# Performance work log

Hardware: AMD Instinct MI355X
Metric: run time of the kernel (lower is better)

The kernel has to match this reference:

```python
import jax, jax.numpy as jnp
import numpy as np

D_MODEL = 512
N_HEADS = 8
D_K = D_MODEL // N_HEADS
D_FF = 2048
N = 4096
EPS = 1e-5


def _layer_norm(x, g, b):
    mu = jnp.mean(x, axis=-1, keepdims=True)
    var = jnp.mean(jnp.square(x - mu), axis=-1, keepdims=True)
    return (x - mu) * jax.lax.rsqrt(var + EPS) * g + b


def setup_inputs() -> dict:
    key = jax.random.key(0)
    ks = jax.random.split(key, 16)
    s = 1.0 / np.sqrt(D_MODEL)
    sf = 1.0 / np.sqrt(D_FF)
    inp = {
        "h": jax.random.normal(ks[0], (N, D_MODEL), dtype=jnp.float32),
        "adj": jax.random.randint(ks[1], (N, N), 0, 2, dtype=jnp.int32),
        "Wq": jax.random.uniform(ks[2], (D_MODEL, D_MODEL), jnp.float32, -s, s),
        "bq": jnp.zeros((D_MODEL,), jnp.float32),
        "Wk": jax.random.uniform(ks[3], (D_MODEL, D_MODEL), jnp.float32, -s, s),
        "bk": jnp.zeros((D_MODEL,), jnp.float32),
        "Wv": jax.random.uniform(ks[4], (D_MODEL, D_MODEL), jnp.float32, -s, s),
        "bv": jnp.zeros((D_MODEL,), jnp.float32),
        "Wo": jax.random.uniform(ks[5], (D_MODEL, D_MODEL), jnp.float32, -s, s),
        "bo": jnp.zeros((D_MODEL,), jnp.float32),
        "W1": jax.random.uniform(ks[6], (D_FF, D_MODEL), jnp.float32, -s, s),
        "b1": jnp.zeros((D_FF,), jnp.float32),
        "W2": jax.random.uniform(ks[7], (D_MODEL, D_FF), jnp.float32, -sf, sf),
        "b2": jnp.zeros((D_MODEL,), jnp.float32),
        "ln1_g": jnp.ones((D_MODEL,), jnp.float32),
        "ln1_b": jnp.zeros((D_MODEL,), jnp.float32),
        "ln2_g": jnp.ones((D_MODEL,), jnp.float32),
        "ln2_b": jnp.zeros((D_MODEL,), jnp.float32),
    }
    return inp


def reference(h, adj, Wq, bq, Wk, bk, Wv, bv, Wo, bo, W1, b1, W2, b2,
              ln1_g, ln1_b, ln2_g, ln2_b):
    n = h.shape[0]
    # adjacency + self loops, used as attention mask (batch=1)
    mask = adj.astype(jnp.float32) + jnp.eye(n, dtype=jnp.float32)  # [N,N]

    # QKV projections, split into heads: [N, H, Dk]
    q = (h @ Wq.T + bq).reshape(n, N_HEADS, D_K)
    k = (h @ Wk.T + bk).reshape(n, N_HEADS, D_K)
    v = (h @ Wv.T + bv).reshape(n, N_HEADS, D_K)

    scores = jnp.einsum("nhd,mhd->hnm", q, k) / jnp.sqrt(jnp.float32(D_K))
    scores = jnp.where(mask[None, :, :] == 0, jnp.float32(-1e9), scores)
    attn = jax.nn.softmax(scores, axis=-1)  # dropout is identity in eval
    ctx = jnp.einsum("hnm,mhd->nhd", attn, v).reshape(n, D_MODEL)
    attn_out = ctx @ Wo.T + bo

    h1 = _layer_norm(h + attn_out, ln1_g, ln1_b)
    ff = jax.nn.relu(h1 @ W1.T + b1) @ W2.T + b2
    h2 = _layer_norm(h1 + ff, ln2_g, ln2_b)
    return h2
```

## Files before the change

kernel.cpp:

```cpp
#include <hip/hip_runtime.h>
#include <stdint.h>
#include <stddef.h>

typedef __bf16 bf16;
typedef __bf16 bf16x8 __attribute__((ext_vector_type(8)));
typedef float  f32x4  __attribute__((ext_vector_type(4)));

typedef __attribute__((address_space(3))) void       lds_void;
typedef __attribute__((address_space(1))) const void gbl_cvoid;

#define ASYNC_CP16(g, l) \
  __builtin_amdgcn_global_load_lds((gbl_cvoid*)(g), (lds_void*)(l), 16, 0, 0)

__device__ __forceinline__ int swz(int r) { return (r & 7) ^ ((r & 8) >> 1); }

struct CastArgs {
  const float* src[7];
  bf16*        dst[7];
  int          cum[8];
};

__global__ __launch_bounds__(256) void k_cast(CastArgs a, int total8)
{
  const int g = blockIdx.x * 256 + threadIdx.x;
  if (g >= total8) return;
  int t = 0;
  while (a.cum[t + 1] <= g) ++t;
  const int i = g - a.cum[t];
  const float4* s = (const float4*)(a.src[t]) + (size_t)i * 2;
  const float4 x0 = s[0], x1 = s[1];
  bf16x8 y;
  y[0] = (bf16)x0.x; y[1] = (bf16)x0.y; y[2] = (bf16)x0.z; y[3] = (bf16)x0.w;
  y[4] = (bf16)x1.x; y[5] = (bf16)x1.y; y[6] = (bf16)x1.z; y[7] = (bf16)x1.w;
  *(bf16x8*)(a.dst[t] + (size_t)i * 8) = y;
}

__device__ __forceinline__ void gemm_core_async(
    const bf16* __restrict__ A, const bf16* __restrict__ B,
    bf16* As, bf16* Bs, f32x4 (&acc)[4][4],
    int K, int m0, int n0, int kbeg, int kend)
{
  const int tid    = threadIdx.x;
  const int lane   = tid & 63;
  const int wave   = tid >> 6;
  const int lane15 = lane & 15;
  const int quad   = lane >> 4;
  const int wm     = (wave & 1) << 6;
  const int wn     = (wave >> 1) << 6;

  int srow[4], soff[4];
#pragma unroll
  for (int i = 0; i < 4; ++i) {
    int c   = ((wave * 4 + i) << 6) + lane;
    srow[i] = c >> 3;
    soff[i] = ((c & 7) ^ swz(srow[i])) * 8;
  }

  const bf16* Ab = A + (size_t)m0 * K;
  const bf16* Bb = B + (size_t)n0 * K;

  for (int k0 = kbeg; k0 < kend; k0 += 64) {
#pragma unroll
    for (int i = 0; i < 4; ++i) {
      ASYNC_CP16(Ab + (size_t)srow[i] * K + k0 + soff[i], &As[(wave * 4 + i) * 512]);
      ASYNC_CP16(Bb + (size_t)srow[i] * K + k0 + soff[i], &Bs[(wave * 4 + i) * 512]);
    }
    __syncthreads();

#pragma unroll
    for (int kk = 0; kk < 2; ++kk) {
      bf16x8 af[4], bfr[4];
#pragma unroll
      for (int f = 0; f < 4; ++f) {
        const int ra = wm + f * 16 + lane15;
        af[f]  = *(const bf16x8*)&As[ra * 64 + (((kk * 4 + quad) ^ swz(ra)) * 8)];
        const int rb = wn + f * 16 + lane15;
        bfr[f] = *(const bf16x8*)&Bs[rb * 64 + (((kk * 4 + quad) ^ swz(rb)) * 8)];
      }
#pragma unroll
      for (int fm = 0; fm < 4; ++fm)
#pragma unroll
        for (int fn = 0; fn < 4; ++fn)
          acc[fm][fn] = __builtin_amdgcn_mfma_f32_16x16x32_bf16(
              af[fm], bfr[fn], acc[fm][fn], 0, 0, 0);
    }
    __syncthreads();
  }
}

__global__ __launch_bounds__(256, 2) void k_gemm(
    const bf16* __restrict__ A, const bf16* __restrict__ B,
    const float* __restrict__ bias, bf16* __restrict__ C,
    int N, int K, int relu)
{
  __shared__ __align__(16) bf16 As[128 * 64];
  __shared__ __align__(16) bf16 Bs[128 * 64];
  const int m0 = blockIdx.x * 128, n0 = blockIdx.y * 128;
  f32x4 acc[4][4] = {};
  gemm_core_async(A, B, As, Bs, acc, K, m0, n0, 0, K);

  const int lane15 = threadIdx.x & 15;
  const int quad   = (threadIdx.x & 63) >> 4;
  const int wave   = threadIdx.x >> 6;
  const int wm     = (wave & 1) << 6, wn = (wave >> 1) << 6;
#pragma unroll
  for (int fm = 0; fm < 4; ++fm)
#pragma unroll
    for (int fn = 0; fn < 4; ++fn) {
      const int col = n0 + wn + fn * 16 + lane15;
      const float bv = bias[col];
#pragma unroll
      for (int r = 0; r < 4; ++r) {
        const int row = m0 + wm + fm * 16 + quad * 4 + r;
        float v = acc[fm][fn][r] + bv;
        if (relu) v = fmaxf(v, 0.0f);
        C[(size_t)row * N + col] = (bf16)v;
      }
    }
}

__global__ __launch_bounds__(256, 2) void k_gemm_qkv(
    const bf16* __restrict__ h,
    const bf16* __restrict__ Wq, const bf16* __restrict__ Wk, const bf16* __restrict__ Wv,
    const float* __restrict__ bq, const float* __restrict__ bk, const float* __restrict__ bv,
    bf16* __restrict__ q, bf16* __restrict__ k, bf16* __restrict__ v)
{
  __shared__ __align__(16) bf16 As[128 * 64];
  __shared__ __align__(16) bf16 Bs[128 * 64];
  const bf16* B; const float* bias; bf16* C;
  if (blockIdx.z == 0)      { B = Wq; bias = bq; C = q; }
  else if (blockIdx.z == 1) { B = Wk; bias = bk; C = k; }
  else                      { B = Wv; bias = bv; C = v; }
  const int m0 = blockIdx.x * 128, n0 = blockIdx.y * 128;
  f32x4 acc[4][4] = {};
  gemm_core_async(h, B, As, Bs, acc, 512, m0, n0, 0, 512);

  const int lane15 = threadIdx.x & 15;
  const int quad   = (threadIdx.x & 63) >> 4;
  const int wave   = threadIdx.x >> 6;
  const int wm     = (wave & 1) << 6, wn = (wave >> 1) << 6;
#pragma unroll
  for (int fm = 0; fm < 4; ++fm)
#pragma unroll
    for (int fn = 0; fn < 4; ++fn) {
      const int col = n0 + wn + fn * 16 + lane15;
      const float bv = bias[col];
#pragma unroll
      for (int r = 0; r < 4; ++r) {
        const int row = m0 + wm + fm * 16 + quad * 4 + r;
        C[(size_t)row * 512 + col] = (bf16)(acc[fm][fn][r] + bv);
      }
    }
}

__global__ __launch_bounds__(256, 2) void k_gemm_sk(
    const bf16* __restrict__ A, const bf16* __restrict__ B,
    float* __restrict__ Cp, int N, int K, int Ksplit)
{
  __shared__ __align__(16) bf16 As[128 * 64];
  __shared__ __align__(16) bf16 Bs[128 * 64];
  const int m0 = blockIdx.x * 128, n0 = blockIdx.y * 128;
  const int kbeg = blockIdx.z * Ksplit;
  f32x4 acc[4][4] = {};
  gemm_core_async(A, B, As, Bs, acc, K, m0, n0, kbeg, kbeg + Ksplit);

  const int lane15 = threadIdx.x & 15;
  const int quad   = (threadIdx.x & 63) >> 4;
  const int wave   = threadIdx.x >> 6;
  const int wm     = (wave & 1) << 6, wn = (wave >> 1) << 6;
  float* Cz = Cp + (size_t)blockIdx.z * 4096 * N;
#pragma unroll
  for (int fm = 0; fm < 4; ++fm)
#pragma unroll
    for (int fn = 0; fn < 4; ++fn) {
      const int col = n0 + wn + fn * 16 + lane15;
#pragma unroll
      for (int r = 0; r < 4; ++r) {
        const int row = m0 + wm + fm * 16 + quad * 4 + r;
        Cz[(size_t)row * N + col] = acc[fm][fn][r];
      }
    }
}

__global__ __launch_bounds__(256) void k_packmask(
    const int* __restrict__ adj, unsigned long long* __restrict__ mb)
{
  const int gw   = (int)((blockIdx.x * 256 + threadIdx.x) >> 6);
  const int lane = threadIdx.x & 63;
  const int a    = adj[(size_t)gw * 64 + lane];
  unsigned long long m = __ballot(a != 0);
  const int row = gw >> 6, wc = gw & 63;
  if ((row >> 6) == wc) m |= 1ull << (row & 63);
  if (lane == 0) mb[gw] = m;
}

__global__ __launch_bounds__(256) void k_transpose_v(
    const bf16* __restrict__ v, bf16* __restrict__ vt)
{
  __shared__ __align__(16) bf16 T[64 * 72];
  const int r0 = blockIdx.x * 64;
  const int c0 = blockIdx.y * 64;
  const int tid = threadIdx.x;
#pragma unroll
  for (int rr = 0; rr < 2; ++rr) {
    int idx = rr * 256 + tid;
    int kr = idx >> 3, ch = (idx & 7) * 8;
    *(bf16x8*)&T[kr * 72 + ch] = *(const bf16x8*)&v[(size_t)(r0 + kr) * 512 + c0 + ch];
  }
  __syncthreads();
#pragma unroll
  for (int rr = 0; rr < 2; ++rr) {
    int idx = rr * 256 + tid;
    int cr = idx >> 3, ch = idx & 7;
    bf16x8 y;
#pragma unroll
    for (int j = 0; j < 8; ++j) y[j] = T[(ch * 8 + j) * 72 + cr];
    *(bf16x8*)&vt[(size_t)(c0 + cr) * 4096 + r0 + ch * 8] = y;
  }
}

__global__ __launch_bounds__(256, 4) void k_attn(
    const bf16* __restrict__ Q, const bf16* __restrict__ Km,
    const bf16* __restrict__ Vt, const unsigned long long* __restrict__ mb,
    bf16* __restrict__ Opart, float* __restrict__ Lpart)
{
  __shared__ __align__(16) bf16 Ks[64 * 72];
  __shared__ __align__(16) bf16 Vs[64 * 72];
  __shared__ __align__(16) bf16 Plb[4][32 * 72];

  const int tid    = threadIdx.x;
  const int wave   = tid >> 6;
  const int lane   = tid & 63;
  const int lane15 = lane & 15;
  const int quad   = lane >> 4;
  const int sp     = blockIdx.x & 3;
  const int hd     = (blockIdx.x >> 2) & 7;
  const int qt     = blockIdx.x >> 5;
  const int qrow   = qt * 128 + wave * 32;

  bf16x8 qf[2][2];
#pragma unroll
  for (int mt = 0; mt < 2; ++mt)
#pragma unroll
    for (int c = 0; c < 2; ++c)
      qf[mt][c] = *(const bf16x8*)&Q[(size_t)(qrow + mt * 16 + lane15) * 512 +
                                     hd * 64 + c * 32 + quad * 8];

  bf16x8 ones;
#pragma unroll
  for (int j = 0; j < 8; ++j) ones[j] = (bf16)1.0f;

  f32x4 o[2][4] = {};
  f32x4 la[2]   = {};

  for (int kt = sp * 16; kt < sp * 16 + 16; ++kt) {
    const int kb = kt * 64;
#pragma unroll
    for (int rr = 0; rr < 2; ++rr) {
      int idx = rr * 256 + tid;
      int a = idx >> 3, ch = (idx & 7) * 8;
      *(bf16x8*)&Ks[a * 72 + ch] = *(const bf16x8*)&Km[(size_t)(kb + a) * 512 + hd * 64 + ch];
      *(bf16x8*)&Vs[a * 72 + ch] = *(const bf16x8*)&Vt[(size_t)(hd * 64 + a) * 4096 + kb + ch];
    }
    __syncthreads();

    unsigned long long mw[2][4];
#pragma unroll
    for (int mt = 0; mt < 2; ++mt)
#pragma unroll
      for (int r = 0; r < 4; ++r)
        mw[mt][r] = mb[(size_t)(qrow + mt * 16 + quad * 4 + r) * 64 + kt] >> lane15;

#pragma unroll
    for (int g = 0; g < 4; ++g) {
      bf16x8 k0f = *(const bf16x8*)&Ks[(g * 16 + lane15) * 72 + quad * 8];
      bf16x8 k1f = *(const bf16x8*)&Ks[(g * 16 + lane15) * 72 + 32 + quad * 8];
#pragma unroll
      for (int mt = 0; mt < 2; ++mt) {
        f32x4 s = {};
        s = __builtin_amdgcn_mfma_f32_16x16x32_bf16(qf[mt][0], k0f, s, 0, 0, 0);
        s = __builtin_amdgcn_mfma_f32_16x16x32_bf16(qf[mt][1], k1f, s, 0, 0, 0);
#pragma unroll
        for (int r = 0; r < 4; ++r) {
          const bool ok = ((mw[mt][r] >> (g * 16)) & 1ull) != 0;
          const float p = ok ? __expf(s[r] * 0.125f) : 0.0f;
          Plb[wave][(mt * 16 + quad * 4 + r) * 72 + g * 16 + lane15] = (bf16)p;
        }
      }
    }

#pragma unroll
    for (int c2 = 0; c2 < 2; ++c2) {
      bf16x8 vf[4];
#pragma unroll
      for (int g2 = 0; g2 < 4; ++g2)
        vf[g2] = *(const bf16x8*)&Vs[(g2 * 16 + lane15) * 72 + c2 * 32 + quad * 8];
#pragma unroll
      for (int mt = 0; mt < 2; ++mt) {
        bf16x8 pa = *(const bf16x8*)&Plb[wave][(mt * 16 + lane15) * 72 + c2 * 32 + quad * 8];
        la[mt] = __builtin_amdgcn_mfma_f32_16x16x32_bf16(pa, ones, la[mt], 0, 0, 0);
#pragma unroll
        for (int g2 = 0; g2 < 4; ++g2)
          o[mt][g2] = __builtin_amdgcn_mfma_f32_16x16x32_bf16(pa, vf[g2], o[mt][g2], 0, 0, 0);
      }
    }
    __syncthreads();
  }

  bf16* Oz = Opart + (size_t)sp * 4096 * 512;
#pragma unroll
  for (int mt = 0; mt < 2; ++mt) {
#pragma unroll
    for (int g2 = 0; g2 < 4; ++g2)
#pragma unroll
      for (int r = 0; r < 4; ++r) {
        const int row = qrow + mt * 16 + quad * 4 + r;
        Oz[(size_t)row * 512 + hd * 64 + g2 * 16 + lane15] = (bf16)o[mt][g2][r];
      }
    if (lane15 == 0) {
#pragma unroll
      for (int r = 0; r < 4; ++r)
        Lpart[sp * 32768 + (qrow + mt * 16 + quad * 4 + r) * 8 + hd] = la[mt][r];
    }
  }
}

__global__ __launch_bounds__(256) void k_attn_combine(
    const bf16* __restrict__ Opart, const float* __restrict__ Lpart,
    bf16* __restrict__ ctx)
{
  const int g = blockIdx.x * 256 + threadIdx.x;
  const size_t base = (size_t)g * 8;
  const int row = g >> 6;
  const int hd  = (g & 63) >> 3;
  float acc[8] = {};
  float l = 0.0f;
#pragma unroll
  for (int s = 0; s < 4; ++s) {
    bf16x8 ov = *(const bf16x8*)&Opart[(size_t)s * 4096 * 512 + base];
#pragma unroll
    for (int j = 0; j < 8; ++j) acc[j] += (float)ov[j];
    l += Lpart[s * 32768 + row * 8 + hd];
  }
  const float rl = 1.0f / l;
  bf16x8 y;
#pragma unroll
  for (int j = 0; j < 8; ++j) y[j] = (bf16)(acc[j] * rl);
  *(bf16x8*)(ctx + base) = y;
}

template <int F32OUT>
__global__ __launch_bounds__(256) void k_addln_sk(
    const bf16* __restrict__ x, const float* __restrict__ Cp,
    const float* __restrict__ bias,
    const float* __restrict__ gam, const float* __restrict__ bet,
    void* __restrict__ out)
{
  const int wave = threadIdx.x >> 6, lane = threadIdx.x & 63;
  const int row  = blockIdx.x * 4 + wave;
  const size_t base = (size_t)row * 512 + lane * 8;
  const int col = lane * 8;
  bf16x8 xv = *(const bf16x8*)(x + base);
  const float* p0 = Cp + base;
  const float* p1 = Cp + (size_t)4096 * 512 + base;
  f32x4 a0 = *(const f32x4*)p0, a1 = *(const f32x4*)(p0 + 4);
  f32x4 b0 = *(const f32x4*)p1, b1 = *(const f32x4*)(p1 + 4);
  f32x4 c0 = *(const f32x4*)(bias + col), c1 = *(const f32x4*)(bias + col + 4);
  float v[8], s = 0.0f, s2 = 0.0f;
#pragma unroll
  for (int j = 0; j < 4; ++j) {
    v[j]     = (float)xv[j]     + a0[j] + b0[j] + c0[j];
    v[4 + j] = (float)xv[4 + j] + a1[j] + b1[j] + c1[j];
  }
#pragma unroll
  for (int j = 0; j < 8; ++j) { s += v[j]; s2 += v[j] * v[j]; }
#pragma unroll
  for (int d = 1; d < 64; d <<= 1) { s += __shfl_xor(s, d, 64); s2 += __shfl_xor(s2, d, 64); }
  const float mu  = s * (1.0f / 512.0f);
  const float var = s2 * (1.0f / 512.0f) - mu * mu;
  const float rs  = rsqrtf(var + 1e-5f);
  f32x4 g0 = *(const f32x4*)(gam + col), g1 = *(const f32x4*)(gam + col + 4);
  f32x4 e0 = *(const f32x4*)(bet + col), e1 = *(const f32x4*)(bet + col + 4);
  if (F32OUT) {
    float* o = (float*)out + base;
#pragma unroll
    for (int j = 0; j < 4; ++j) {
      o[j]     = ((v[j] - mu) * rs) * g0[j] + e0[j];
      o[4 + j] = ((v[4 + j] - mu) * rs) * g1[j] + e1[j];
    }
  } else {
    bf16x8 ov;
#pragma unroll
    for (int j = 0; j < 4; ++j) {
      ov[j]     = (bf16)(((v[j] - mu) * rs) * g0[j] + e0[j]);
      ov[4 + j] = (bf16)(((v[4 + j] - mu) * rs) * g1[j] + e1[j]);
    }
    *(bf16x8*)((bf16*)out + base) = ov;
  }
}

extern "C" void kernel_launch(void* const* d_in, const int* in_sizes, int n_in,
                              void* d_out, int out_size, void* d_ws, size_t ws_size,
                              hipStream_t stream)
{
  const int*   adj = (const int*)  d_in[1];
  const float* bq  = (const float*)d_in[3];
  const float* bk  = (const float*)d_in[5];
  const float* bv  = (const float*)d_in[7];
  const float* bo  = (const float*)d_in[9];
  const float* b1  = (const float*)d_in[11];
  const float* b2  = (const float*)d_in[13];
  const float* g1  = (const float*)d_in[14];
  const float* be1 = (const float*)d_in[15];
  const float* g2  = (const float*)d_in[16];
  const float* be2 = (const float*)d_in[17];

  char* ws = (char*)d_ws;
  const size_t MB = 1024 * 1024;

  bf16* hb  = (bf16*)(ws + 0 * MB);
  bf16* Wqb = (bf16*)(ws + 4 * MB);
  bf16* Wkb = (bf16*)(ws + 4 * MB + 512 * 1024);
  bf16* Wvb = (bf16*)(ws + 5 * MB);
  bf16* Wob = (bf16*)(ws + 5 * MB + 512 * 1024);
  bf16* W1b = (bf16*)(ws + 6 * MB);
  bf16* W2b = (bf16*)(ws + 8 * MB);

  bf16* q    = (bf16*)(ws + 12 * MB);
  bf16* k    = (bf16*)(ws + 16 * MB);
  bf16* v    = (bf16*)(ws + 20 * MB);
  bf16* vt   = (bf16*)(ws + 24 * MB);
  unsigned long long* mbits = (unsigned long long*)(ws + 28 * MB);
  bf16* ctx  = (bf16*)(ws + 30 * MB);
  bf16*  Opart = (bf16*)(ws + 34 * MB);
  float* Lpart = (float*)(ws + 50 * MB);
  float* skP   = (float*)(ws + 34 * MB);
  bf16* h1   = (bf16*)(ws + 12 * MB);
  bf16* ff1  = (bf16*)(ws + 16 * MB);

  CastArgs ca;
  const int srcIdx[7] = {0, 2, 4, 6, 8, 10, 12};
  bf16* dsts[7] = {hb, Wqb, Wkb, Wvb, Wob, W1b, W2b};
  int cum = 0;
  for (int t = 0; t < 7; ++t) {
    ca.src[t] = (const float*)d_in[srcIdx[t]];
    ca.dst[t] = dsts[t];
    ca.cum[t] = cum;
    cum += in_sizes[srcIdx[t]] / 8;
  }
  ca.cum[7] = cum;

  const dim3 blk(256);
  k_cast<<<dim3((cum + 255) / 256), blk, 0, stream>>>(ca, cum);

  k_gemm_qkv<<<dim3(32, 4, 3), blk, 0, stream>>>(hb, Wqb, Wkb, Wvb, bq, bk, bv, q, k, v);
  k_transpose_v<<<dim3(64, 8), blk, 0, stream>>>(v, vt);
  k_packmask<<<dim3(65536), blk, 0, stream>>>(adj, mbits);
  k_attn<<<dim3(1024), blk, 0, stream>>>(q, k, vt, mbits, Opart, Lpart);
  k_attn_combine<<<dim3(1024), blk, 0, stream>>>(Opart, Lpart, ctx);
  k_gemm_sk<<<dim3(32, 4, 2), blk, 0, stream>>>(ctx, Wob, skP, 512, 512, 256);
  k_addln_sk<0><<<dim3(1024), blk, 0, stream>>>(hb, skP, bo, g1, be1, (void*)h1);
  k_gemm<<<dim3(32, 16), blk, 0, stream>>>(h1, W1b, b1, ff1, 2048, 512, 1);
  k_gemm_sk<<<dim3(32, 4, 2), blk, 0, stream>>>(ff1, W2b, skP, 512, 2048, 1024);
  k_addln_sk<1><<<dim3(1024), blk, 0, stream>>>(h1, skP, b2, g2, be2, d_out);
}
```

Before: 311.8 us.

## Fuse prep kernels, fold V transpose into QKV GEMM, use async loads in attention

Merges the mask packing and fp32->bf16 cast into one launch. Treats Wq/Wk/Wv as one concatenated weight matrix (relying on their contiguous workspace layout) in a 64-row-tile QKV GEMM whose V epilogue writes the transposed V directly, which removes the separate transpose kernel. The split-K GEMMs move to 64-row tiles with higher occupancy, and attention now loads K/V tiles into swizzled LDS with async global-to-LDS copies. Together these cut launch count and extra global traffic, at the cost of smaller tiles with less reuse.

```diff
diff --git a/kernel.cpp b/kernel.cpp
--- a/kernel.cpp
+++ b/kernel.cpp
@@ -20,40 +20,62 @@
   int          cum[8];
 };
 
-__global__ __launch_bounds__(256) void k_cast(CastArgs a, int total8)
-{
-  const int g = blockIdx.x * 256 + threadIdx.x;
-  if (g >= total8) return;
-  int t = 0;
-  while (a.cum[t + 1] <= g) ++t;
-  const int i = g - a.cum[t];
-  const float4* s = (const float4*)(a.src[t]) + (size_t)i * 2;
-  const float4 x0 = s[0], x1 = s[1];
-  bf16x8 y;
-  y[0] = (bf16)x0.x; y[1] = (bf16)x0.y; y[2] = (bf16)x0.z; y[3] = (bf16)x0.w;
-  y[4] = (bf16)x1.x; y[5] = (bf16)x1.y; y[6] = (bf16)x1.z; y[7] = (bf16)x1.w;
-  *(bf16x8*)(a.dst[t] + (size_t)i * 8) = y;
-}
-
+__global__ __launch_bounds__(256) void k_prep(
+    const int* __restrict__ adj, unsigned long long* __restrict__ mb,
+    CastArgs a, int total8)
+{
+  const int bid = blockIdx.x;
+  if (bid < 65536) {
+    const int gw   = (int)(((unsigned)bid * 256 + threadIdx.x) >> 6);
+    const int lane = threadIdx.x & 63;
+    const int av   = adj[(size_t)gw * 64 + lane];
+    unsigned long long m = __ballot(av != 0);
+    const int row = gw >> 6, wc = gw & 63;
+    if ((row >> 6) == wc) m |= 1ull << (row & 63);
+    if (lane == 0) mb[gw] = m;
+  } else {
+    const int g = (bid - 65536) * 256 + threadIdx.x;
+    if (g >= total8) return;
+    int t = 0;
+    while (a.cum[t + 1] <= g) ++t;
+    const int i = g - a.cum[t];
+    const float4* s = (const float4*)(a.src[t]) + (size_t)i * 2;
+    const float4 x0 = s[0], x1 = s[1];
+    bf16x8 y;
+    y[0] = (bf16)x0.x; y[1] = (bf16)x0.y; y[2] = (bf16)x0.z; y[3] = (bf16)x0.w;
+    y[4] = (bf16)x1.x; y[5] = (bf16)x1.y; y[6] = (bf16)x1.z; y[7] = (bf16)x1.w;
+    *(bf16x8*)(a.dst[t] + (size_t)i * 8) = y;
+  }
+}
+
+template <int MT>
 __device__ __forceinline__ void gemm_core_async(
     const bf16* __restrict__ A, const bf16* __restrict__ B,
-    bf16* As, bf16* Bs, f32x4 (&acc)[4][4],
+    bf16* As, bf16* Bs, f32x4 (&acc)[4][(MT == 128) ? 4 : 2],
     int K, int m0, int n0, int kbeg, int kend)
 {
+  constexpr int FN = (MT == 128) ? 4 : 2;
+  constexpr int IA = MT / 32;
   const int tid    = threadIdx.x;
   const int lane   = tid & 63;
   const int wave   = tid >> 6;
   const int lane15 = lane & 15;
   const int quad   = lane >> 4;
-  const int wm     = (wave & 1) << 6;
-  const int wn     = (wave >> 1) << 6;
-
-  int srow[4], soff[4];
+  const int wm     = (MT == 128) ? ((wave & 1) << 6) : 0;
+  const int wn     = (MT == 128) ? ((wave >> 1) << 6) : (wave << 5);
+
+  int srA[IA], soA[IA], srB[4], soB[4];
+#pragma unroll
+  for (int i = 0; i < IA; ++i) {
+    int c  = ((wave * IA + i) << 6) + lane;
+    srA[i] = c >> 3;
+    soA[i] = ((c & 7) ^ swz(srA[i])) * 8;
+  }
 #pragma unroll
   for (int i = 0; i < 4; ++i) {
-    int c   = ((wave * 4 + i) << 6) + lane;
-    srow[i] = c >> 3;
-    soff[i] = ((c & 7) ^ swz(srow[i])) * 8;
+    int c  = ((wave * 4 + i) << 6) + lane;
+    srB[i] = c >> 3;
+    soB[i] = ((c & 7) ^ swz(srB[i])) * 8;
   }
 
   const bf16* Ab = A + (size_t)m0 * K;
@@ -61,26 +83,30 @@
 
   for (int k0 = kbeg; k0 < kend; k0 += 64) {
 #pragma unroll
-    for (int i = 0; i < 4; ++i) {
-      ASYNC_CP16(Ab + (size_t)srow[i] * K + k0 + soff[i], &As[(wave * 4 + i) * 512]);
-      ASYNC_CP16(Bb + (size_t)srow[i] * K + k0 + soff[i], &Bs[(wave * 4 + i) * 512]);
-    }
+    for (int i = 0; i < IA; ++i)
+      ASYNC_CP16(Ab + (size_t)srA[i] * K + k0 + soA[i], &As[(wave * IA + i) * 512]);
+#pragma unroll
+    for (int i = 0; i < 4; ++i)
+      ASYNC_CP16(Bb + (size_t)srB[i] * K + k0 + soB[i], &Bs[(wave * 4 + i) * 512]);
     __syncthreads();
 
 #pragma unroll
     for (int kk = 0; kk < 2; ++kk) {
-      bf16x8 af[4], bfr[4];
+      bf16x8 af[4], bfr[FN];
 #pragma unroll
       for (int f = 0; f < 4; ++f) {
         const int ra = wm + f * 16 + lane15;
-        af[f]  = *(const bf16x8*)&As[ra * 64 + (((kk * 4 + quad) ^ swz(ra)) * 8)];
+        af[f] = *(const bf16x8*)&As[ra * 64 + (((kk * 4 + quad) ^ swz(ra)) * 8)];
+      }
+#pragma unroll
+      for (int f = 0; f < FN; ++f) {
         const int rb = wn + f * 16 + lane15;
         bfr[f] = *(const bf16x8*)&Bs[rb * 64 + (((kk * 4 + quad) ^ swz(rb)) * 8)];
       }
 #pragma unroll
       for (int fm = 0; fm < 4; ++fm)
 #pragma unroll
-        for (int fn = 0; fn < 4; ++fn)
+        for (int fn = 0; fn < FN; ++fn)
           acc[fm][fn] = __builtin_amdgcn_mfma_f32_16x16x32_bf16(
               af[fm], bfr[fn], acc[fm][fn], 0, 0, 0);
     }
@@ -97,12 +123,12 @@
   __shared__ __align__(16) bf16 Bs[128 * 64];
   const int m0 = blockIdx.x * 128, n0 = blockIdx.y * 128;
   f32x4 acc[4][4] = {};
-  gemm_core_async(A, B, As, Bs, acc, K, m0, n0, 0, K);
+  gemm_core_async<128>(A, B, As, Bs, acc, K, m0, n0, 0, K);
 
   const int lane15 = threadIdx.x & 15;
   const int quad   = (threadIdx.x & 63) >> 4;
   const int wave   = threadIdx.x >> 6;
-  const int wm     = (wave & 1) << 6, wn = (wave >> 1) << 6;
+  const int wm = (wave & 1) << 6, wn = (wave >> 1) << 6;
 #pragma unroll
   for (int fm = 0; fm < 4; ++fm)
 #pragma unroll
@@ -119,104 +145,93 @@
     }
 }
 
-__global__ __launch_bounds__(256, 2) void k_gemm_qkv(
-    const bf16* __restrict__ h,
-    const bf16* __restrict__ Wq, const bf16* __restrict__ Wk, const bf16* __restrict__ Wv,
-    const float* __restrict__ bq, const float* __restrict__ bk, const float* __restrict__ bv,
-    bf16* __restrict__ q, bf16* __restrict__ k, bf16* __restrict__ v)
-{
-  __shared__ __align__(16) bf16 As[128 * 64];
-  __shared__ __align__(16) bf16 Bs[128 * 64];
-  const bf16* B; const float* bias; bf16* C;
-  if (blockIdx.z == 0)      { B = Wq; bias = bq; C = q; }
-  else if (blockIdx.z == 1) { B = Wk; bias = bk; C = k; }
-  else                      { B = Wv; bias = bv; C = v; }
-  const int m0 = blockIdx.x * 128, n0 = blockIdx.y * 128;
-  f32x4 acc[4][4] = {};
-  gemm_core_async(h, B, As, Bs, acc, 512, m0, n0, 0, 512);
+__global__ __launch_bounds__(256, 4) void k_gemm_qkv(
+    const bf16* __restrict__ h, const bf16* __restrict__ Wcat,
+    const float* __restrict__ bq, const float* __restrict__ bk,
+    const float* __restrict__ bv,
+    bf16* __restrict__ q, bf16* __restrict__ k, bf16* __restrict__ vt)
+{
+  __shared__ __align__(16) bf16 SM[64 * 64 + 128 * 64];
+  bf16* As = SM;
+  bf16* Bs = SM + 64 * 64;
+  const int m0 = blockIdx.x * 64, n0 = blockIdx.y * 128;
+  f32x4 acc[4][2] = {};
+  gemm_core_async<64>(h, Wcat, As, Bs, acc, 512, m0, n0, 0, 512);
 
   const int lane15 = threadIdx.x & 15;
   const int quad   = (threadIdx.x & 63) >> 4;
   const int wave   = threadIdx.x >> 6;
-  const int wm     = (wave & 1) << 6, wn = (wave >> 1) << 6;
-#pragma unroll
-  for (int fm = 0; fm < 4; ++fm)
-#pragma unroll
-    for (int fn = 0; fn < 4; ++fn) {
-      const int col = n0 + wn + fn * 16 + lane15;
-      const float bv = bias[col];
-#pragma unroll
-      for (int r = 0; r < 4; ++r) {
-        const int row = m0 + wm + fm * 16 + quad * 4 + r;
-        C[(size_t)row * 512 + col] = (bf16)(acc[fm][fn][r] + bv);
-      }
-    }
-}
-
-__global__ __launch_bounds__(256, 2) void k_gemm_sk(
+  const int wn     = wave << 5;
+  const int proj   = n0 >> 9;
+  const int ncol0  = n0 & 511;
+  const float* bias = (proj == 0) ? bq : (proj == 1) ? bk : bv;
+
+  if (proj < 2) {
+    bf16* C = proj ? k : q;
+#pragma unroll
+    for (int fm = 0; fm < 4; ++fm)
+#pragma unroll
+      for (int fn = 0; fn < 2; ++fn) {
+        const int col = ncol0 + wn + fn * 16 + lane15;
+        const float bvv = bias[col];
+#pragma unroll
+        for (int r = 0; r < 4; ++r) {
+          const int row = m0 + fm * 16 + quad * 4 + r;
+          C[(size_t)row * 512 + col] = (bf16)(acc[fm][fn][r] + bvv);
+        }
+      }
+  } else {
+    __syncthreads();
+#pragma unroll
+    for (int fm = 0; fm < 4; ++fm)
+#pragma unroll
+      for (int fn = 0; fn < 2; ++fn) {
+        const int colL = wn + fn * 16 + lane15;
+        const float bvv = bias[ncol0 + colL];
+#pragma unroll
+        for (int r = 0; r < 4; ++r) {
+          const int rowL = fm * 16 + quad * 4 + r;
+          SM[colL * 72 + rowL] = (bf16)(acc[fm][fn][r] + bvv);
+        }
+      }
+    __syncthreads();
+#pragma unroll
+    for (int i = 0; i < 4; ++i) {
+      const int c = i * 256 + threadIdx.x;
+      const int colL = c >> 3, rw = (c & 7) * 8;
+      *(bf16x8*)&vt[(size_t)(ncol0 + colL) * 4096 + m0 + rw] =
+          *(const bf16x8*)&SM[colL * 72 + rw];
+    }
+  }
+}
+
+__global__ __launch_bounds__(256, 4) void k_gemm_sk(
     const bf16* __restrict__ A, const bf16* __restrict__ B,
     float* __restrict__ Cp, int N, int K, int Ksplit)
 {
-  __shared__ __align__(16) bf16 As[128 * 64];
+  __shared__ __align__(16) bf16 As[64 * 64];
   __shared__ __align__(16) bf16 Bs[128 * 64];
-  const int m0 = blockIdx.x * 128, n0 = blockIdx.y * 128;
+  const int m0 = blockIdx.x * 64, n0 = blockIdx.y * 128;
   const int kbeg = blockIdx.z * Ksplit;
-  f32x4 acc[4][4] = {};
-  gemm_core_async(A, B, As, Bs, acc, K, m0, n0, kbeg, kbeg + Ksplit);
+  f32x4 acc[4][2] = {};
+  gemm_core_async<64>(A, B, As, Bs, acc, K, m0, n0, kbeg, kbeg + Ksplit);
 
   const int lane15 = threadIdx.x & 15;
   const int quad   = (threadIdx.x & 63) >> 4;
   const int wave   = threadIdx.x >> 6;
-  const int wm     = (wave & 1) << 6, wn = (wave >> 1) << 6;
+  const int wn     = wave << 5;
   float* Cz = Cp + (size_t)blockIdx.z * 4096 * N;
 #pragma unroll
   for (int fm = 0; fm < 4; ++fm)
 #pragma unroll
-    for (int fn = 0; fn < 4; ++fn) {
+    for (int fn = 0; fn < 2; ++fn) {
       const int col = n0 + wn + fn * 16 + lane15;
 #pragma unroll
       for (int r = 0; r < 4; ++r) {
-        const int row = m0 + wm + fm * 16 + quad * 4 + r;
+        const int row = m0 + fm * 16 + quad * 4 + r;
         Cz[(size_t)row * N + col] = acc[fm][fn][r];
       }
     }
-}
-
-__global__ __launch_bounds__(256) void k_packmask(
-    const int* __restrict__ adj, unsigned long long* __restrict__ mb)
-{
-  const int gw   = (int)((blockIdx.x * 256 + threadIdx.x) >> 6);
-  const int lane = threadIdx.x & 63;
-  const int a    = adj[(size_t)gw * 64 + lane];
-  unsigned long long m = __ballot(a != 0);
-  const int row = gw >> 6, wc = gw & 63;
-  if ((row >> 6) == wc) m |= 1ull << (row & 63);
-  if (lane == 0) mb[gw] = m;
-}
-
-__global__ __launch_bounds__(256) void k_transpose_v(
-    const bf16* __restrict__ v, bf16* __restrict__ vt)
-{
-  __shared__ __align__(16) bf16 T[64 * 72];
-  const int r0 = blockIdx.x * 64;
-  const int c0 = blockIdx.y * 64;
-  const int tid = threadIdx.x;
-#pragma unroll
-  for (int rr = 0; rr < 2; ++rr) {
-    int idx = rr * 256 + tid;
-    int kr = idx >> 3, ch = (idx & 7) * 8;
-    *(bf16x8*)&T[kr * 72 + ch] = *(const bf16x8*)&v[(size_t)(r0 + kr) * 512 + c0 + ch];
-  }
-  __syncthreads();
-#pragma unroll
-  for (int rr = 0; rr < 2; ++rr) {
-    int idx = rr * 256 + tid;
-    int cr = idx >> 3, ch = idx & 7;
-    bf16x8 y;
-#pragma unroll
-    for (int j = 0; j < 8; ++j) y[j] = T[(ch * 8 + j) * 72 + cr];
-    *(bf16x8*)&vt[(size_t)(c0 + cr) * 4096 + r0 + ch * 8] = y;
-  }
 }
 
 __global__ __launch_bounds__(256, 4) void k_attn(
@@ -224,8 +239,8 @@
     const bf16* __restrict__ Vt, const unsigned long long* __restrict__ mb,
     bf16* __restrict__ Opart, float* __restrict__ Lpart)
 {
-  __shared__ __align__(16) bf16 Ks[64 * 72];
-  __shared__ __align__(16) bf16 Vs[64 * 72];
+  __shared__ __align__(16) bf16 Ks[64 * 64];
+  __shared__ __align__(16) bf16 Vs[64 * 64];
   __shared__ __align__(16) bf16 Plb[4][32 * 72];
 
   const int tid    = threadIdx.x;
@@ -246,6 +261,20 @@
       qf[mt][c] = *(const bf16x8*)&Q[(size_t)(qrow + mt * 16 + lane15) * 512 +
                                      hd * 64 + c * 32 + quad * 8];
 
+  int srK[2], soK[2];
+#pragma unroll
+  for (int i = 0; i < 2; ++i) {
+    int c  = ((wave * 2 + i) << 6) + lane;
+    srK[i] = c >> 3;
+    soK[i] = ((c & 7) ^ swz(srK[i])) * 8;
+  }
+  const bf16* KmB[2] = {
+      Km + (size_t)srK[0] * 512 + hd * 64 + soK[0],
+      Km + (size_t)srK[1] * 512 + hd * 64 + soK[1]};
+  const bf16* VtB[2] = {
+      Vt + (size_t)(hd * 64 + srK[0]) * 4096 + soK[0],
+      Vt + (size_t)(hd * 64 + srK[1]) * 4096 + soK[1]};
+
   bf16x8 ones;
 #pragma unroll
   for (int j = 0; j < 8; ++j) ones[j] = (bf16)1.0f;
@@ -256,11 +285,9 @@
   for (int kt = sp * 16; kt < sp * 16 + 16; ++kt) {
     const int kb = kt * 64;
 #pragma unroll
-    for (int rr = 0; rr < 2; ++rr) {
-      int idx = rr * 256 + tid;
-      int a = idx >> 3, ch = (idx & 7) * 8;
-      *(bf16x8*)&Ks[a * 72 + ch] = *(const bf16x8*)&Km[(size_t)(kb + a) * 512 + hd * 64 + ch];
-      *(bf16x8*)&Vs[a * 72 + ch] = *(const bf16x8*)&Vt[(size_t)(hd * 64 + a) * 4096 + kb + ch];
+    for (int i = 0; i < 2; ++i) {
+      ASYNC_CP16(KmB[i] + (size_t)kb * 512, &Ks[(wave * 2 + i) * 512]);
+      ASYNC_CP16(VtB[i] + kb,               &Vs[(wave * 2 + i) * 512]);
     }
     __syncthreads();
 
@@ -273,8 +300,9 @@
 
 #pragma unroll
     for (int g = 0; g < 4; ++g) {
-      bf16x8 k0f = *(const bf16x8*)&Ks[(g * 16 + lane15) * 72 + quad * 8];
-      bf16x8 k1f = *(const bf16x8*)&Ks[(g * 16 + lane15) * 72 + 32 + quad * 8];
+      const int row = g * 16 + lane15;
+      bf16x8 k0f = *(const bf16x8*)&Ks[row * 64 + ((quad       ^ swz(row)) * 8)];
+      bf16x8 k1f = *(const bf16x8*)&Ks[row * 64 + (((4 + quad) ^ swz(row)) * 8)];
 #pragma unroll
       for (int mt = 0; mt < 2; ++mt) {
         f32x4 s = {};
@@ -293,8 +321,10 @@
     for (int c2 = 0; c2 < 2; ++c2) {
       bf16x8 vf[4];
 #pragma unroll
-      for (int g2 = 0; g2 < 4; ++g2)
-        vf[g2] = *(const bf16x8*)&Vs[(g2 * 16 + lane15) * 72 + c2 * 32 + quad * 8];
+      for (int g2 = 0; g2 < 4; ++g2) {
+        const int row = g2 * 16 + lane15;
+        vf[g2] = *(const bf16x8*)&Vs[row * 64 + (((c2 * 4 + quad) ^ swz(row)) * 8)];
+      }
 #pragma unroll
       for (int mt = 0; mt < 2; ++mt) {
         bf16x8 pa = *(const bf16x8*)&Plb[wave][(mt * 16 + lane15) * 72 + c2 * 32 + quad * 8];
@@ -428,7 +458,6 @@
 
   bf16* q    = (bf16*)(ws + 12 * MB);
   bf16* k    = (bf16*)(ws + 16 * MB);
-  bf16* v    = (bf16*)(ws + 20 * MB);
   bf16* vt   = (bf16*)(ws + 24 * MB);
   unsigned long long* mbits = (unsigned long long*)(ws + 28 * MB);
   bf16* ctx  = (bf16*)(ws + 30 * MB);
@@ -451,16 +480,14 @@
   ca.cum[7] = cum;
 
   const dim3 blk(256);
-  k_cast<<<dim3((cum + 255) / 256), blk, 0, stream>>>(ca, cum);
-
-  k_gemm_qkv<<<dim3(32, 4, 3), blk, 0, stream>>>(hb, Wqb, Wkb, Wvb, bq, bk, bv, q, k, v);
-  k_transpose_v<<<dim3(64, 8), blk, 0, stream>>>(v, vt);
-  k_packmask<<<dim3(65536), blk, 0, stream>>>(adj, mbits);
+
+  k_prep<<<dim3(65536 + (cum + 255) / 256), blk, 0, stream>>>(adj, mbits, ca, cum);
+  k_gemm_qkv<<<dim3(64, 12), blk, 0, stream>>>(hb, Wqb, bq, bk, bv, q, k, vt);
   k_attn<<<dim3(1024), blk, 0, stream>>>(q, k, vt, mbits, Opart, Lpart);
   k_attn_combine<<<dim3(1024), blk, 0, stream>>>(Opart, Lpart, ctx);
-  k_gemm_sk<<<dim3(32, 4, 2), blk, 0, stream>>>(ctx, Wob, skP, 512, 512, 256);
+  k_gemm_sk<<<dim3(64, 4, 2), blk, 0, stream>>>(ctx, Wob, skP, 512, 512, 256);
   k_addln_sk<0><<<dim3(1024), blk, 0, stream>>>(hb, skP, bo, g1, be1, (void*)h1);
   k_gemm<<<dim3(32, 16), blk, 0, stream>>>(h1, W1b, b1, ff1, 2048, 512, 1);
-  k_gemm_sk<<<dim3(32, 4, 2), blk, 0, stream>>>(ff1, W2b, skP, 512, 2048, 1024);
+  k_gemm_sk<<<dim3(64, 4, 2), blk, 0, stream>>>(ff1, W2b, skP, 512, 2048, 1024);
   k_addln_sk<1><<<dim3(1024), blk, 0, stream>>>(h1, skP, b2, g2, be2, d_out);
 }
```

After: 290.5 us. -6.8%, faster.
